# Optimization experiments

Measured on AMD Instinct MI355X. Metric: run time of the kernel, lower is better.

## Reference

```python
import jax, jax.numpy as jnp
import numpy as np

S, M, B, D, H, DH = 1024, 1024, 4, 1024, 16, 64
T = S + M


def _rel_shift(x):
    # x: [i, j, b, n] -> Transformer-XL relative shift
    i, j = x.shape[0], x.shape[1]
    zero_pad = jnp.zeros((i, 1) + x.shape[2:], x.dtype)
    x_padded = jnp.concatenate([zero_pad, x], axis=1)
    x_padded = x_padded.reshape((j + 1, i) + x.shape[2:])
    return x_padded[1:].reshape(x.shape)


def setup_inputs() -> dict:
    key = jax.random.key(0)
    ks = jax.random.split(key, 8)
    sc = 0.02
    x = jax.random.normal(ks[0], (S, B, D), jnp.float32)
    memory = jax.random.normal(ks[1], (M, B, D), jnp.float32)
    pos_emb = jax.random.normal(ks[2], (T, D), jnp.float32)
    pos_bias_u = jax.random.normal(ks[3], (H, DH), jnp.float32) * sc
    pos_bias_v = jax.random.normal(ks[4], (H, DH), jnp.float32) * sc
    W_qkv = jax.random.normal(ks[5], (D, 3 * H * DH), jnp.float32) * sc
    W_rel = jax.random.normal(ks[6], (D, H * DH), jnp.float32) * sc
    W_o = jax.random.normal(ks[7], (H * DH, D), jnp.float32) * sc
    gamma = jnp.ones((D,), jnp.float32)
    beta = jnp.zeros((D,), jnp.float32)
    # causal mask accounting for memory: query i attends keys j <= i + M
    causal = jnp.arange(T)[None, :] > (jnp.arange(S)[:, None] + M)
    mask = jnp.broadcast_to(causal[:, :, None], (S, T, B))
    return {"x": x, "pos_emb": pos_emb, "pos_bias_u": pos_bias_u,
            "pos_bias_v": pos_bias_v, "memory": memory,
            "W_qkv": W_qkv, "W_rel": W_rel, "W_o": W_o,
            "gamma": gamma, "beta": beta, "mask": mask}


def reference(x, pos_emb, pos_bias_u, pos_bias_v, memory, W_qkv, W_rel, W_o, gamma, beta, mask):
    seq_len, batch, d_model = x.shape
    num_head, d_head = pos_bias_u.shape
    scale = 1.0 / d_head ** 0.5

    c = jnp.concatenate([memory, x], axis=0)          # [T, B, D]
    total_len = c.shape[0]

    qkv = c @ W_qkv                                   # [T, B, 3*H*DH]
    q, k, v = jnp.split(qkv, 3, axis=-1)
    q = q.reshape(total_len, batch, num_head, d_head)[-seq_len:]  # [S,B,H,DH]
    k = k.reshape(total_len, batch, num_head, d_head)             # [T,B,H,DH]
    v = v.reshape(total_len, batch, num_head, d_head)             # [T,B,H,DH]
    r = (pos_emb @ W_rel).reshape(total_len, num_head, d_head)    # [T,H,DH]

    AC = jnp.einsum('ibnd,jbnd->ijbn', q + pos_bias_u, k)  # content-content
    BD = jnp.einsum('ibnd,jnd->ijbn', q + pos_bias_v, r)   # content-position
    BD = _rel_shift(BD)

    attn_score = (AC + BD) * scale                    # [S,T,B,H]
    attn_score = jnp.where(mask[:, :, :, None], -jnp.inf, attn_score)
    attn_prob = jax.nn.softmax(attn_score, axis=1)

    attn_vec = jnp.einsum('ijbn,jbnd->ibnd', attn_prob, v)
    attn_vec = attn_vec.reshape(seq_len, batch, num_head * d_head)
    attn_out = attn_vec @ W_o                         # [S,B,D]

    y = x + attn_out
    mu = jnp.mean(y, axis=-1, keepdims=True)
    var = jnp.var(y, axis=-1, keepdims=True)
    return (y - mu) / jnp.sqrt(var + 1e-5) * gamma + beta
```

## Files before the change

### kernel.cpp

```cpp
#include <hip/hip_runtime.h>
#include <math.h>
#include <cstdint>
#include <cstddef>


typedef _Float16 half_t;
typedef _Float16 half8 __attribute__((ext_vector_type(8)));
typedef _Float16 half4v __attribute__((ext_vector_type(4)));
typedef float f32x4 __attribute__((ext_vector_type(4)));

#define S_LEN 1024
#define M_LEN 1024
#define T_LEN 2048
#define BATCH 4
#define NHEAD 16

__device__ inline void async_copy16(const half_t* g, half_t* l) {
  __builtin_amdgcn_global_load_lds(
      (const __attribute__((address_space(1))) void*)g,
      (__attribute__((address_space(3))) void*)l, 16, 0, 0);
}

__global__ __launch_bounds__(256) void k_convert3(const float* __restrict__ mem,
                                                  const float* __restrict__ x,
                                                  const float* __restrict__ pos,
                                                  half_t* __restrict__ cbf,
                                                  half_t* __restrict__ posb) {
  const int i = blockIdx.x * 256 + threadIdx.x;
  const float* src;
  half_t* dst;
  int off;
  if (i < 1048576)      { src = mem; dst = cbf;           off = i; }
  else if (i < 2097152) { src = x;   dst = cbf + 4194304; off = i - 1048576; }
  else                  { src = pos; dst = posb;          off = i - 2097152; }
  const float4 v = ((const float4*)src)[off];
  half4v h;
  h[0] = (half_t)v.x; h[1] = (half_t)v.y; h[2] = (half_t)v.z; h[3] = (half_t)v.w;
  ((half4v*)dst)[off] = h;
}

__global__ __launch_bounds__(256) void k_transpose_w3(const float* __restrict__ Wqkv,
                                                      const float* __restrict__ Wrel,
                                                      const float* __restrict__ Wo,
                                                      half_t* __restrict__ wqkvT,
                                                      half_t* __restrict__ wrelT,
                                                      half_t* __restrict__ woT) {
  __shared__ float tile[64][65];
  const int y = blockIdx.y;
  const float* src; half_t* dst; int C, c0;
  if (y < 48)      { src = Wqkv; dst = wqkvT; C = 3072; c0 = y * 64; }
  else if (y < 64) { src = Wrel; dst = wrelT; C = 1024; c0 = (y - 48) * 64; }
  else             { src = Wo;   dst = woT;   C = 1024; c0 = (y - 64) * 64; }
  const int t = threadIdx.x;
  const int r0 = blockIdx.x * 64;
  const int tx = t & 63, ty4 = t >> 6;
#pragma unroll
  for (int k = 0; k < 16; ++k) {
    int row = k * 4 + ty4;
    tile[row][tx] = src[(size_t)(r0 + row) * C + c0 + tx];
  }
  __syncthreads();
#pragma unroll
  for (int k = 0; k < 16; ++k) {
    int orow = k * 4 + ty4;
    dst[(size_t)(c0 + orow) * 1024 + r0 + tx] = (half_t)tile[tx][orow];
  }
}

__device__ inline void gemm_body(const half_t* __restrict__ A,
                                 const half_t* __restrict__ B,
                                 half_t* __restrict__ C,
                                 int N, int K, int m0, int n0,
                                 half_t (*ldsA)[64], half_t (*ldsB)[64]) {
  const int t = threadIdx.x;
  const int wave = t >> 6, lane = t & 63, quad = lane >> 4, l15 = lane & 15;
  const int wm = (wave >> 1) * 64, wn = (wave & 1) * 64;
  const int srow = lane >> 3;
  const int scol = ((lane & 7) ^ srow) * 8;
  f32x4 acc[4][4] = {};
  for (int k0 = 0; k0 < K; k0 += 64) {
    __syncthreads();
#pragma unroll
    for (int i = 0; i < 4; ++i) {
      const int r0 = (wave * 4 + i) * 8;
      async_copy16(&A[(size_t)(m0 + r0 + srow) * K + k0 + scol], &ldsA[r0][0]);
      async_copy16(&B[(size_t)(n0 + r0 + srow) * K + k0 + scol], &ldsB[r0][0]);
    }
    __syncthreads();
#pragma unroll
    for (int ks = 0; ks < 2; ++ks) {
      half8 af[4], bf[4];
#pragma unroll
      for (int mt = 0; mt < 4; ++mt)
        af[mt] = *(const half8*)&ldsA[wm + mt * 16 + l15][((ks * 4 + quad) ^ (l15 & 7)) * 8];
#pragma unroll
      for (int nt = 0; nt < 4; ++nt)
        bf[nt] = *(const half8*)&ldsB[wn + nt * 16 + l15][((ks * 4 + quad) ^ (l15 & 7)) * 8];
#pragma unroll
      for (int mt = 0; mt < 4; ++mt)
#pragma unroll
        for (int nt = 0; nt < 4; ++nt)
          acc[mt][nt] = __builtin_amdgcn_mfma_f32_16x16x32_f16(af[mt], bf[nt], acc[mt][nt], 0, 0, 0);
    }
  }
#pragma unroll
  for (int mt = 0; mt < 4; ++mt)
#pragma unroll
    for (int nt = 0; nt < 4; ++nt)
#pragma unroll
      for (int r = 0; r < 4; ++r) {
        const int row = m0 + wm + mt * 16 + quad * 4 + r;
        const int col = n0 + wn + nt * 16 + l15;
        C[(size_t)row * N + col] = (half_t)acc[mt][nt][r];
      }
}

__global__ __launch_bounds__(256) void k_gemm(const half_t* __restrict__ A,
                                              const half_t* __restrict__ B,
                                              half_t* __restrict__ C,
                                              int M, int N, int K) {
  __shared__ half_t ldsA[128][64];
  __shared__ half_t ldsB[128][64];
  gemm_body(A, B, C, N, K, blockIdx.x * 128, blockIdx.y * 128, ldsA, ldsB);
}

__global__ __launch_bounds__(256) void k_gemm_qkv_pos(const half_t* __restrict__ cbf,
                                                      const half_t* __restrict__ wqkvT,
                                                      half_t* __restrict__ qkv,
                                                      const half_t* __restrict__ posb,
                                                      const half_t* __restrict__ wrelT,
                                                      half_t* __restrict__ rb) {
  __shared__ half_t ldsA[128][64];
  __shared__ half_t ldsB[128][64];
  const int bid = blockIdx.x;
  if (bid < 1536)
    gemm_body(cbf, wqkvT, qkv, 3072, 1024, (bid & 63) * 128, (bid >> 6) * 128, ldsA, ldsB);
  else {
    const int b2 = bid - 1536;
    gemm_body(posb, wrelT, rb, 1024, 1024, (b2 & 15) * 128, (b2 >> 4) * 128, ldsA, ldsB);
  }
}

__global__ __launch_bounds__(256) void k_transpose_v(const half_t* __restrict__ qkv,
                                                     half_t* __restrict__ vT) {
  __shared__ half_t tile[64][72];
  const int t = threadIdx.x;
  const int t0 = blockIdx.x * 64, bn = blockIdx.y, b = bn >> 4, n = bn & 15;
#pragma unroll
  for (int i = 0; i < 2; ++i) {
    const int ci = t + i * 256;
    const int row = ci >> 3, co = (ci & 7) * 8;
    *(half8*)&tile[row][co] =
        *(const half8*)&qkv[((size_t)(t0 + row) * BATCH + b) * 3072 + 2048 + n * 64 + co];
  }
  __syncthreads();
#pragma unroll
  for (int i = 0; i < 2; ++i) {
    const int ci = t + i * 256;
    const int dh = ci >> 3, to = (ci & 7) * 8;
    half8 v;
#pragma unroll
    for (int j = 0; j < 8; ++j) v[j] = tile[to + j][dh];
    *(half8*)&vT[((size_t)bn * 64 + dh) * 2048 + t0 + to] = v;
  }
}

__global__ __launch_bounds__(512, 4) void k_attn(const half_t* __restrict__ qkv,
                                                 const half_t* __restrict__ rbuf,
                                                 const half_t* __restrict__ vT,
                                                 const float* __restrict__ pbu,
                                                 const float* __restrict__ pbv,
                                                 half_t* __restrict__ av) {
  __shared__ __align__(16) half_t ldsK[64][64];
  __shared__ __align__(16) half_t ldsV[64][64];
  __shared__ __align__(16) half_t ldsR[192][64];
  __shared__ __align__(16) half_t ldsEP[8][16][120];
  const int t = threadIdx.x;
  const int wave = t >> 6, lane = t & 63, quad = lane >> 4, l15 = lane & 15;

  const int li = blockIdx.x + 8 * blockIdx.y;
  const int c = li & 255, kr = li >> 8;
  const int xe = kr == 0 ? (c & 7) : 7 - (c & 7);
  const int bn = (c >> 3) + (kr << 5);
  const int i0 = xe * 128;
  const int b = bn >> 4, n = bn & 15;
  const int i_base = i0 + wave * 16;
  const int rbase = 112 - wave * 16;

  half8 qu[2], qv[2];
#pragma unroll
  for (int ks = 0; ks < 2; ++ks) {
    const int dh0 = ks * 32 + quad * 8;
    const half8 qf = *(const half8*)&qkv[((size_t)(M_LEN + i_base + l15) * BATCH + b) * 3072 + n * 64 + dh0];
#pragma unroll
    for (int j = 0; j < 8; ++j) {
      const float qj = (float)qf[j];
      qu[ks][j] = (half_t)(qj + pbu[n * 64 + dh0 + j]);
      qv[ks][j] = (half_t)(qj + pbv[n * 64 + dh0 + j]);
    }
  }

  f32x4 oacc[4] = {};
  float lpart[4] = {0.f, 0.f, 0.f, 0.f};
  const float k1 = 0.125f * 1.44269504088896f;
  const float kC = -4.0f * 1.44269504088896f;

  const int srow = t >> 3, sc3 = t & 7;
  const int sxk = (sc3 ^ (srow & 7)) * 8;
  int rrow[3], rc3[3];
#pragma unroll
  for (int i = 0; i < 3; ++i) {
    const int ci = t + 512 * i;
    rrow[i] = ci >> 3; rc3[i] = ci & 7;
  }

  const int ntile = xe * 2 + 18;

  half8 kreg = *(const half8*)&qkv[((size_t)srow * BATCH + b) * 3072 + 1024 + n * 64 + sc3 * 8];
  half8 vreg = *(const half8*)&vT[((size_t)bn * 64 + srow) * 2048 + sc3 * 8];
  half8 rreg[3];
#pragma unroll
  for (int i = 0; i < 3; ++i) {
    int p = 896 - i0 + rrow[i];
    p = p > 2047 ? 2047 : p;
    rreg[i] = *(const half8*)&rbuf[(size_t)p * 1024 + n * 64 + rc3[i] * 8];
  }

  for (int kt = 0; kt < ntile; ++kt) {
    const int j0 = kt * 64;

    __syncthreads();
    *(half8*)&ldsK[srow][sxk] = kreg;
    *(half8*)&ldsV[srow][sxk] = vreg;
#pragma unroll
    for (int i = 0; i < 3; ++i)
      *(half8*)&ldsR[rrow[i]][((rc3[i] ^ (rrow[i] & 7)) * 8)] = rreg[i];
    __syncthreads();

    if (kt + 1 < ntile) {
      const int j0n = j0 + 64;
      kreg = *(const half8*)&qkv[((size_t)(j0n + srow) * BATCH + b) * 3072 + 1024 + n * 64 + sc3 * 8];
      vreg = *(const half8*)&vT[((size_t)bn * 64 + srow) * 2048 + j0n + sc3 * 8];
      const int p_lo = j0n + 896 - i0;
#pragma unroll
      for (int i = 0; i < 3; ++i) {
        int p = p_lo + rrow[i];
        p = p > 2047 ? 2047 : p;
        rreg[i] = *(const half8*)&rbuf[(size_t)p * 1024 + n * 64 + rc3[i] * 8];
      }
    }

    f32x4 ac[4] = {};
#pragma unroll
    for (int ks = 0; ks < 2; ++ks)
#pragma unroll
      for (int nt = 0; nt < 4; ++nt) {
        const int row = nt * 16 + l15;
        const half8 kf = *(const half8*)&ldsK[row][((ks * 4 + quad) ^ (row & 7)) * 8];
        ac[nt] = __builtin_amdgcn_mfma_f32_16x16x32_f16(qu[ks], kf, ac[nt], 0, 0, 0);
      }

    f32x4 ea[5] = {};
#pragma unroll
    for (int ks = 0; ks < 2; ++ks)
#pragma unroll
      for (int et = 0; et < 5; ++et) {
        const int row = rbase + et * 16 + l15;
        const half8 rf = *(const half8*)&ldsR[row][((ks * 4 + quad) ^ (row & 7)) * 8];
        ea[et] = __builtin_amdgcn_mfma_f32_16x16x32_f16(qv[ks], rf, ea[et], 0, 0, 0);
      }
#pragma unroll
    for (int et = 0; et < 5; ++et)
#pragma unroll
      for (int r = 0; r < 4; ++r) {
        const int row = quad * 4 + r;
        ldsEP[wave][row][et * 16 + l15 + row + ((row & 12) << 1)] = (half_t)ea[et][r];
      }
    __builtin_amdgcn_wave_barrier();

    const bool maskt = j0 > i_base + 960;
#pragma unroll
    for (int r = 0; r < 4; ++r) {
      const int irow = quad * 4 + r;
      const int ig = i_base + irow;
      const int swz = (irow & 12) << 1;
      float ev[4];
#pragma unroll
      for (int nt = 0; nt < 4; ++nt)
        ev[nt] = (float)ldsEP[wave][irow][nt * 16 + l15 + 15 + swz];
      float psum = 0.f;
#pragma unroll
      for (int nt = 0; nt < 4; ++nt) {
        const int cj = nt * 16 + l15;
        float p = __builtin_amdgcn_exp2f(fmaf(ac[nt][r] + ev[nt], k1, kC));
        if (maskt && (j0 + cj > ig + M_LEN)) p = 0.f;
        psum += p;
        ldsEP[wave][irow][cj + swz] = (half_t)p;
      }
      lpart[r] += psum;
    }
    __builtin_amdgcn_wave_barrier();

    half8 pa[2];
#pragma unroll
    for (int ks = 0; ks < 2; ++ks)
      pa[ks] = *(const half8*)&ldsEP[wave][l15][ks * 32 + quad * 8 + ((l15 & 12) << 1)];
#pragma unroll
    for (int ks = 0; ks < 2; ++ks)
#pragma unroll
      for (int dnt = 0; dnt < 4; ++dnt) {
        const int row = dnt * 16 + l15;
        const half8 vf = *(const half8*)&ldsV[row][((ks * 4 + quad) ^ (row & 7)) * 8];
        oacc[dnt] = __builtin_amdgcn_mfma_f32_16x16x32_f16(pa[ks], vf, oacc[dnt], 0, 0, 0);
      }
  }

#pragma unroll
  for (int r = 0; r < 4; ++r) {
    float l = lpart[r];
#pragma unroll
    for (int off = 1; off < 16; off <<= 1) l += __shfl_xor(l, off);
    const float inv = 1.0f / l;
    const int ig = i_base + quad * 4 + r;
#pragma unroll
    for (int dnt = 0; dnt < 4; ++dnt)
      av[((size_t)ig * BATCH + b) * 1024 + n * 64 + dnt * 16 + l15] = (half_t)(oacc[dnt][r] * inv);
  }
}

__global__ __launch_bounds__(256) void k_ln(const float* __restrict__ x,
                                            const half_t* __restrict__ ao,
                                            const float* __restrict__ gamma,
                                            const float* __restrict__ beta,
                                            float* __restrict__ out) {
  const int row = blockIdx.x;
  const int t = threadIdx.x;
  const float4 xv = ((const float4*)(x + (size_t)row * 1024))[t];
  const half4v a4 = ((const half4v*)(ao + (size_t)row * 1024))[t];
  const float y0 = xv.x + (float)a4[0];
  const float y1 = xv.y + (float)a4[1];
  const float y2 = xv.z + (float)a4[2];
  const float y3 = xv.w + (float)a4[3];
  float s = y0 + y1 + y2 + y3;
  float ss = y0 * y0 + y1 * y1 + y2 * y2 + y3 * y3;
#pragma unroll
  for (int off = 1; off < 64; off <<= 1) {
    s += __shfl_xor(s, off);
    ss += __shfl_xor(ss, off);
  }
  __shared__ float sb[4], ssb[4];
  if ((t & 63) == 0) { sb[t >> 6] = s; ssb[t >> 6] = ss; }
  __syncthreads();
  s = sb[0] + sb[1] + sb[2] + sb[3];
  ss = ssb[0] + ssb[1] + ssb[2] + ssb[3];
  const float mean = s * (1.f / 1024.f);
  const float var = ss * (1.f / 1024.f) - mean * mean;
  const float rstd = rsqrtf(var + 1e-5f);
  const float4 g = ((const float4*)gamma)[t];
  const float4 be = ((const float4*)beta)[t];
  float4 o;
  o.x = (y0 - mean) * rstd * g.x + be.x;
  o.y = (y1 - mean) * rstd * g.y + be.y;
  o.z = (y2 - mean) * rstd * g.z + be.z;
  o.w = (y3 - mean) * rstd * g.w + be.w;
  ((float4*)(out + (size_t)row * 1024))[t] = o;
}

extern "C" void kernel_launch(void* const* d_in, const int* in_sizes, int n_in,
                              void* d_out, int out_size, void* d_ws, size_t ws_size,
                              hipStream_t stream) {
  const float* x     = (const float*)d_in[0];
  const float* pos   = (const float*)d_in[1];
  const float* pbu   = (const float*)d_in[2];
  const float* pbv   = (const float*)d_in[3];
  const float* mem   = (const float*)d_in[4];
  const float* Wqkv  = (const float*)d_in[5];
  const float* Wrel  = (const float*)d_in[6];
  const float* Wo    = (const float*)d_in[7];
  const float* gamma = (const float*)d_in[8];
  const float* beta  = (const float*)d_in[9];
  float* out = (float*)d_out;

  half_t* ws    = (half_t*)d_ws;
  half_t* cbf   = ws;
  half_t* posb  = cbf + 8388608;
  half_t* wqkvT = posb + 2097152;
  half_t* wrelT = wqkvT + 3145728;
  half_t* woT   = wrelT + 1048576;
  half_t* qkv   = woT + 1048576;
  half_t* rb    = qkv + 25165824;
  half_t* vT    = rb + 2097152;
  half_t* av    = vT + 8388608;
  half_t* aout  = qkv;

  k_convert3<<<10240, 256, 0, stream>>>(mem, x, pos, cbf, posb);
  k_transpose_w3<<<dim3(16, 80), 256, 0, stream>>>(Wqkv, Wrel, Wo, wqkvT, wrelT, woT);
  k_gemm_qkv_pos<<<1664, 256, 0, stream>>>(cbf, wqkvT, qkv, posb, wrelT, rb);
  k_transpose_v<<<dim3(32, 64), 256, 0, stream>>>(qkv, vT);
  k_attn<<<dim3(8, 64), 512, 0, stream>>>(qkv, rb, vT, pbu, pbv, av);
  k_gemm<<<dim3(32, 8), 256, 0, stream>>>(av, woT, aout, 4096, 1024, 1024);
  k_ln<<<4096, 256, 0, stream>>>(x, aout, gamma, beta, out);
}
```

Before: 342.8 us.

## Use ring buffer for R tiles in attention and split-K output projection

The attention kernel now keeps position-embedding rows in a 256-row circular LDS buffer, so each key tile loads only 64 new R rows per thread instead of reloading all 192 rows. The output projection GEMM is split along K into two halves, launched as 512 blocks instead of 256 so more CUs are busy. The two partial results are written to separate fp16 buffers and summed in the LayerNorm kernel. This adds LDS usage, a second rounding of partial sums to fp16, and extra reads in LayerNorm. The kt==0 path also carries a redundant scalar store.

```diff
diff --git a/kernel.cpp b/kernel.cpp
--- a/kernel.cpp
+++ b/kernel.cpp
@@ -70,7 +70,7 @@
 __device__ inline void gemm_body(const half_t* __restrict__ A,
                                  const half_t* __restrict__ B,
                                  half_t* __restrict__ C,
-                                 int N, int K, int m0, int n0,
+                                 int N, int K, int ld, int m0, int n0,
                                  half_t (*ldsA)[64], half_t (*ldsB)[64]) {
   const int t = threadIdx.x;
   const int wave = t >> 6, lane = t & 63, quad = lane >> 4, l15 = lane & 15;
@@ -83,8 +83,8 @@
 #pragma unroll
     for (int i = 0; i < 4; ++i) {
       const int r0 = (wave * 4 + i) * 8;
-      async_copy16(&A[(size_t)(m0 + r0 + srow) * K + k0 + scol], &ldsA[r0][0]);
-      async_copy16(&B[(size_t)(n0 + r0 + srow) * K + k0 + scol], &ldsB[r0][0]);
+      async_copy16(&A[(size_t)(m0 + r0 + srow) * ld + k0 + scol], &ldsA[r0][0]);
+      async_copy16(&B[(size_t)(n0 + r0 + srow) * ld + k0 + scol], &ldsB[r0][0]);
     }
     __syncthreads();
 #pragma unroll
@@ -113,15 +113,6 @@
         const int col = n0 + wn + nt * 16 + l15;
         C[(size_t)row * N + col] = (half_t)acc[mt][nt][r];
       }
-}
-
-__global__ __launch_bounds__(256) void k_gemm(const half_t* __restrict__ A,
-                                              const half_t* __restrict__ B,
-                                              half_t* __restrict__ C,
-                                              int M, int N, int K) {
-  __shared__ half_t ldsA[128][64];
-  __shared__ half_t ldsB[128][64];
-  gemm_body(A, B, C, N, K, blockIdx.x * 128, blockIdx.y * 128, ldsA, ldsB);
 }
 
 __global__ __launch_bounds__(256) void k_gemm_qkv_pos(const half_t* __restrict__ cbf,
@@ -134,11 +125,23 @@
   __shared__ half_t ldsB[128][64];
   const int bid = blockIdx.x;
   if (bid < 1536)
-    gemm_body(cbf, wqkvT, qkv, 3072, 1024, (bid & 63) * 128, (bid >> 6) * 128, ldsA, ldsB);
+    gemm_body(cbf, wqkvT, qkv, 3072, 1024, 1024, (bid & 63) * 128, (bid >> 6) * 128, ldsA, ldsB);
   else {
     const int b2 = bid - 1536;
-    gemm_body(posb, wrelT, rb, 1024, 1024, (b2 & 15) * 128, (b2 >> 4) * 128, ldsA, ldsB);
-  }
+    gemm_body(posb, wrelT, rb, 1024, 1024, 1024, (b2 & 15) * 128, (b2 >> 4) * 128, ldsA, ldsB);
+  }
+}
+
+__global__ __launch_bounds__(256) void k_gemm_proj(const half_t* __restrict__ av,
+                                                   const half_t* __restrict__ woT,
+                                                   half_t* __restrict__ out0,
+                                                   half_t* __restrict__ out1) {
+  __shared__ half_t ldsA[128][64];
+  __shared__ half_t ldsB[128][64];
+  const int bid = blockIdx.x;
+  const int h = bid >> 8, b2 = bid & 255;
+  gemm_body(av + h * 512, woT + h * 512, h ? out1 : out0,
+            1024, 512, 1024, (b2 & 31) * 128, (b2 >> 5) * 128, ldsA, ldsB);
 }
 
 __global__ __launch_bounds__(256) void k_transpose_v(const half_t* __restrict__ qkv,
@@ -173,7 +176,7 @@
                                                  half_t* __restrict__ av) {
   __shared__ __align__(16) half_t ldsK[64][64];
   __shared__ __align__(16) half_t ldsV[64][64];
-  __shared__ __align__(16) half_t ldsR[192][64];
+  __shared__ __align__(16) half_t ldsR[256][64];
   __shared__ __align__(16) half_t ldsEP[8][16][120];
   const int t = threadIdx.x;
   const int wave = t >> 6, lane = t & 63, quad = lane >> 4, l15 = lane & 15;
@@ -185,7 +188,7 @@
   const int i0 = xe * 128;
   const int b = bn >> 4, n = bn & 15;
   const int i_base = i0 + wave * 16;
-  const int rbase = 112 - wave * 16;
+  const int p0 = 896 - i0;
 
   half8 qu[2], qv[2];
 #pragma unroll
@@ -207,24 +210,21 @@
 
   const int srow = t >> 3, sc3 = t & 7;
   const int sxk = (sc3 ^ (srow & 7)) * 8;
-  int rrow[3], rc3[3];
-#pragma unroll
-  for (int i = 0; i < 3; ++i) {
-    const int ci = t + 512 * i;
-    rrow[i] = ci >> 3; rc3[i] = ci & 7;
-  }
 
   const int ntile = xe * 2 + 18;
 
   half8 kreg = *(const half8*)&qkv[((size_t)srow * BATCH + b) * 3072 + 1024 + n * 64 + sc3 * 8];
   half8 vreg = *(const half8*)&vT[((size_t)bn * 64 + srow) * 2048 + sc3 * 8];
-  half8 rreg[3];
-#pragma unroll
-  for (int i = 0; i < 3; ++i) {
-    int p = 896 - i0 + rrow[i];
-    p = p > 2047 ? 2047 : p;
-    rreg[i] = *(const half8*)&rbuf[(size_t)p * 1024 + n * 64 + rc3[i] * 8];
-  }
+  half8 rreg4[4];
+  int rr4[4], rc4[4];
+#pragma unroll
+  for (int i = 0; i < 4; ++i) {
+    const int ci = t + 512 * i;
+    rr4[i] = ci >> 3; rc4[i] = ci & 7;
+    const int ps = p0 + rr4[i] > 2047 ? 2047 : p0 + rr4[i];
+    rreg4[i] = *(const half8*)&rbuf[(size_t)ps * 1024 + n * 64 + rc4[i] * 8];
+  }
+  half8 rpre;
 
   for (int kt = 0; kt < ntile; ++kt) {
     const int j0 = kt * 64;
@@ -232,22 +232,26 @@
     __syncthreads();
     *(half8*)&ldsK[srow][sxk] = kreg;
     *(half8*)&ldsV[srow][sxk] = vreg;
-#pragma unroll
-    for (int i = 0; i < 3; ++i)
-      *(half8*)&ldsR[rrow[i]][((rc3[i] ^ (rrow[i] & 7)) * 8)] = rreg[i];
+    if (kt == 0) {
+#pragma unroll
+      for (int i = 0; i < 4; ++i) {
+        const int pg = p0 + rr4[i];
+        ldsR[pg & 255][(rc4[i] ^ (pg & 7)) * 8] = rreg4[i][0];
+        *(half8*)&ldsR[pg & 255][(rc4[i] ^ (pg & 7)) * 8] = rreg4[i];
+      }
+    } else {
+      const int pw = j0 + p0 + 192 + srow;
+      *(half8*)&ldsR[pw & 255][(sc3 ^ (pw & 7)) * 8] = rpre;
+    }
     __syncthreads();
 
     if (kt + 1 < ntile) {
       const int j0n = j0 + 64;
       kreg = *(const half8*)&qkv[((size_t)(j0n + srow) * BATCH + b) * 3072 + 1024 + n * 64 + sc3 * 8];
       vreg = *(const half8*)&vT[((size_t)bn * 64 + srow) * 2048 + j0n + sc3 * 8];
-      const int p_lo = j0n + 896 - i0;
-#pragma unroll
-      for (int i = 0; i < 3; ++i) {
-        int p = p_lo + rrow[i];
-        p = p > 2047 ? 2047 : p;
-        rreg[i] = *(const half8*)&rbuf[(size_t)p * 1024 + n * 64 + rc3[i] * 8];
-      }
+      const int pn = j0 + p0 + 256 + srow;
+      const int pc = pn > 2047 ? 2047 : pn;
+      rpre = *(const half8*)&rbuf[(size_t)pc * 1024 + n * 64 + sc3 * 8];
     }
 
     f32x4 ac[4] = {};
@@ -260,13 +264,14 @@
         ac[nt] = __builtin_amdgcn_mfma_f32_16x16x32_f16(qu[ks], kf, ac[nt], 0, 0, 0);
       }
 
+    const int rbg = j0 + p0 + 112 - wave * 16;
     f32x4 ea[5] = {};
 #pragma unroll
     for (int ks = 0; ks < 2; ++ks)
 #pragma unroll
       for (int et = 0; et < 5; ++et) {
-        const int row = rbase + et * 16 + l15;
-        const half8 rf = *(const half8*)&ldsR[row][((ks * 4 + quad) ^ (row & 7)) * 8];
+        const int pr = rbg + et * 16 + l15;
+        const half8 rf = *(const half8*)&ldsR[pr & 255][((ks * 4 + quad) ^ (pr & 7)) * 8];
         ea[et] = __builtin_amdgcn_mfma_f32_16x16x32_f16(qv[ks], rf, ea[et], 0, 0, 0);
       }
 #pragma unroll
@@ -329,18 +334,20 @@
 }
 
 __global__ __launch_bounds__(256) void k_ln(const float* __restrict__ x,
-                                            const half_t* __restrict__ ao,
+                                            const half_t* __restrict__ ao0,
+                                            const half_t* __restrict__ ao1,
                                             const float* __restrict__ gamma,
                                             const float* __restrict__ beta,
                                             float* __restrict__ out) {
   const int row = blockIdx.x;
   const int t = threadIdx.x;
   const float4 xv = ((const float4*)(x + (size_t)row * 1024))[t];
-  const half4v a4 = ((const half4v*)(ao + (size_t)row * 1024))[t];
-  const float y0 = xv.x + (float)a4[0];
-  const float y1 = xv.y + (float)a4[1];
-  const float y2 = xv.z + (float)a4[2];
-  const float y3 = xv.w + (float)a4[3];
+  const half4v a4 = ((const half4v*)(ao0 + (size_t)row * 1024))[t];
+  const half4v b4 = ((const half4v*)(ao1 + (size_t)row * 1024))[t];
+  const float y0 = xv.x + (float)a4[0] + (float)b4[0];
+  const float y1 = xv.y + (float)a4[1] + (float)b4[1];
+  const float y2 = xv.z + (float)a4[2] + (float)b4[2];
+  const float y3 = xv.w + (float)a4[3] + (float)b4[3];
   float s = y0 + y1 + y2 + y3;
   float ss = y0 * y0 + y1 * y1 + y2 * y2 + y3 * y3;
 #pragma unroll
@@ -391,13 +398,14 @@
   half_t* rb    = qkv + 25165824;
   half_t* vT    = rb + 2097152;
   half_t* av    = vT + 8388608;
-  half_t* aout  = qkv;
+  half_t* aout0 = qkv;
+  half_t* aout1 = qkv + 4194304;
 
   k_convert3<<<10240, 256, 0, stream>>>(mem, x, pos, cbf, posb);
   k_transpose_w3<<<dim3(16, 80), 256, 0, stream>>>(Wqkv, Wrel, Wo, wqkvT, wrelT, woT);
   k_gemm_qkv_pos<<<1664, 256, 0, stream>>>(cbf, wqkvT, qkv, posb, wrelT, rb);
   k_transpose_v<<<dim3(32, 64), 256, 0, stream>>>(qkv, vT);
   k_attn<<<dim3(8, 64), 512, 0, stream>>>(qkv, rb, vT, pbu, pbv, av);
-  k_gemm<<<dim3(32, 8), 256, 0, stream>>>(av, woT, aout, 4096, 1024, 1024);
-  k_ln<<<4096, 256, 0, stream>>>(x, aout, gamma, beta, out);
-}
+  k_gemm_proj<<<512, 256, 0, stream>>>(av, woT, aout0, aout1);
+  k_ln<<<4096, 256, 0, stream>>>(x, aout0, aout1, gamma, beta, out);
+}
```

Result: faster. 332.1 us (-3.1%).
